# Kernel tuning notes

Measured on AMD Instinct MI355X. Metric: run time of the kernel, lower is better.

The kernel has to match this reference:

```python
import jax, jax.numpy as jnp
import numpy as np

NUM_HEADS = 16

def setup_inputs() -> dict:
    key = jax.random.key(0)
    k1, k2, k3 = jax.random.split(key, 3)
    T, B, E = 2048, 4, 1024
    x = jax.random.normal(k1, (T, B, E), dtype=jnp.float32)
    # xavier-ish scaled weights
    in_proj_w = jax.random.normal(k2, (3 * E, E), dtype=jnp.float32) * (1.0 / np.sqrt(E))
    in_proj_b = jnp.zeros((3 * E,), dtype=jnp.float32)
    out_w = jax.random.normal(k3, (E, E), dtype=jnp.float32) * (1.0 / np.sqrt(E))
    out_b = jnp.zeros((E,), dtype=jnp.float32)
    return {"x": x, "in_proj_w": in_proj_w, "in_proj_b": in_proj_b,
            "out_w": out_w, "out_b": out_b}

def reference(x, in_proj_w, in_proj_b, out_w, out_b):
    # Self-attention (query=key=value=x), shapes: x [T, B, E]
    T, B, E = x.shape
    H = NUM_HEADS
    D = E // H
    scaling = D ** -0.5
    # fused QKV projection: [T, B, 3E]
    qkv = jnp.einsum('tbe,fe->tbf', x, in_proj_w) + in_proj_b
    q, k, v = jnp.split(qkv, 3, axis=-1)
    q = q * scaling
    # [T, B, E] -> [B, H, T, D]
    def to_heads(t):
        return t.reshape(T, B, H, D).transpose(1, 2, 0, 3)
    q, k, v = to_heads(q), to_heads(k), to_heads(v)
    # scores [B, H, T, T], softmax in float32 as in the original
    scores = jnp.einsum('bhtd,bhsd->bhts', q, k)
    attn_weights = jax.nn.softmax(scores.astype(jnp.float32), axis=-1).astype(scores.dtype)
    # attn [B, H, T, D] -> [T, B, E]
    attn = jnp.einsum('bhts,bhsd->bhtd', attn_weights, v)
    attn = attn.transpose(2, 0, 1, 3).reshape(T, B, E)
    out = jnp.einsum('tbe,fe->tbf', attn, out_w) + out_b
    # averaged attention weights over heads: [B, T, T]
    avg_weights = attn_weights.sum(axis=1) / H
    return out, avg_weights
```

## Files before the change

### kernel.cpp

```cpp
#include <hip/hip_runtime.h>
#include <hip/hip_bf16.h>
#include <cstdint>
#include <cstddef>

typedef __attribute__((ext_vector_type(8))) short s16x8;
typedef __attribute__((ext_vector_type(4))) float f32x4;
typedef __attribute__((ext_vector_type(8))) float f32x8;
typedef __attribute__((ext_vector_type(8))) _Float16 h8;
typedef __attribute__((ext_vector_type(4))) _Float16 h4;

#define TT 2048
#define BB 4
#define EE 1024
#define HH 16
#define DD 64
#define MR 8192

#define MFMA_BF16(a,b,c) __builtin_amdgcn_mfma_f32_16x16x32_bf16(a,b,c,0,0,0)
#define MFMA_F16(a,b,c)  __builtin_amdgcn_mfma_f32_16x16x32_f16(a,b,c,0,0,0)

__device__ __forceinline__ ushort f2bf(float f) {
  uint32_t u = __float_as_uint(f);
  u += 0x7fffu + ((u >> 16) & 1u);
  return (ushort)(u >> 16);
}

#define GL2L(g, l) __builtin_amdgcn_global_load_lds( \
    (__attribute__((address_space(1))) void*)(g), \
    (__attribute__((address_space(3))) void*)(l), 16, 0, 0)

__global__ void cast_f32_bf16(const float* __restrict__ in, ushort* __restrict__ out, int n4) {
  int stride = gridDim.x * blockDim.x;
  for (int i = blockIdx.x * blockDim.x + threadIdx.x; i < n4; i += stride) {
    float4 v = ((const float4*)in)[i];
    ushort4 o;
    o.x = f2bf(v.x); o.y = f2bf(v.y); o.z = f2bf(v.z); o.w = f2bf(v.w);
    ((ushort4*)out)[i] = o;
  }
}

__global__ __launch_bounds__(256) void gemm_qkv(
    const ushort* __restrict__ A, const ushort* __restrict__ W,
    const float* __restrict__ bias,
    ushort* __restrict__ Qb, ushort* __restrict__ Kb, ushort* __restrict__ Vt)
{
  __shared__ ushort As[128 * 32];
  __shared__ ushort Bs[128 * 32];
  const int K = EE;
  int tid = threadIdx.x;
  int bn = blockIdx.x, bm = blockIdx.y;
  int brow = bm * 128, bcol = bn * 128;
  int lane = tid & 63, wid = tid >> 6;
  int wm = wid >> 1, wn = wid & 1;
  int lr = lane & 15, kg = lane >> 4;

  f32x4 zero = {0.f, 0.f, 0.f, 0.f};
  f32x4 acc[4][4];
#pragma unroll
  for (int i = 0; i < 4; i++)
#pragma unroll
    for (int j = 0; j < 4; j++) acc[i][j] = zero;

  int r0 = tid >> 2, c0 = (tid & 3) * 8;
  const ushort* Abase = A + (size_t)brow * K;
  const ushort* Wbase = W + (size_t)bcol * K;

  for (int k0 = 0; k0 < K; k0 += 32) {
    __syncthreads();
    GL2L(Abase + (size_t)r0 * K + k0 + c0,        &As[tid * 8]);
    GL2L(Abase + (size_t)(r0 + 64) * K + k0 + c0, &As[(tid + 256) * 8]);
    GL2L(Wbase + (size_t)r0 * K + k0 + c0,        &Bs[tid * 8]);
    GL2L(Wbase + (size_t)(r0 + 64) * K + k0 + c0, &Bs[(tid + 256) * 8]);
    __syncthreads();
    s16x8 af[4], bfr[4];
#pragma unroll
    for (int i = 0; i < 4; i++) af[i]  = *(const s16x8*)&As[(wm * 64 + i * 16 + lr) * 32 + kg * 8];
#pragma unroll
    for (int j = 0; j < 4; j++) bfr[j] = *(const s16x8*)&Bs[(wn * 64 + j * 16 + lr) * 32 + kg * 8];
#pragma unroll
    for (int i = 0; i < 4; i++)
#pragma unroll
      for (int j = 0; j < 4; j++)
        acc[i][j] = MFMA_BF16(af[i], bfr[j], acc[i][j]);
  }

#pragma unroll
  for (int i = 0; i < 4; i++)
#pragma unroll
    for (int j = 0; j < 4; j++) {
      int n = bcol + wn * 64 + j * 16 + lr;
      float bv = bias[n];
      int sec = n >> 10;
      int hd = n & 1023;
      int h = hd >> 6, d = hd & 63;
#pragma unroll
      for (int e = 0; e < 4; e++) {
        int m = brow + wm * 64 + i * 16 + kg * 4 + e;
        int t = m >> 2, b = m & 3;
        float v = acc[i][j][e] + bv;
        size_t hoff = (size_t)(b * HH + h);
        if (sec == 0)      Qb[(hoff * TT + t) * DD + d] = f2bf(v * 0.125f);
        else if (sec == 1) Kb[(hoff * TT + t) * DD + d] = f2bf(v);
        else { _Float16 hv = (_Float16)v; Vt[(hoff * DD + d) * TT + t] = *(ushort*)&hv; }
      }
    }
}

__global__ __launch_bounds__(512, 2) void attn_fused(
    const ushort* __restrict__ Qb, const ushort* __restrict__ Kb,
    const _Float16* __restrict__ Vt, ushort* __restrict__ attn,
    float* __restrict__ avgp)
{
  __shared__ _Float16 sc[32 * 2048];
  __shared__ float scr[2048];
  __shared__ float invl[32];

  const int qt = blockIdx.x;
  const int b  = blockIdx.y;
  const int tid = threadIdx.x;
  const int lane = tid & 63;
  const int w = tid >> 6;
  const int m = lane & 15;
  const int kq = lane >> 4;
  const int t0 = qt * 32;

  f32x8 av[4][4];
#pragma unroll
  for (int u = 0; u < 4; u++)
#pragma unroll
    for (int c = 0; c < 4; c++) av[u][c] = (f32x8)(0.f);

  for (int h = 0; h < HH; ++h) {
    const size_t bh = (size_t)b * HH + h;

    const ushort* qp = Qb + (bh * TT + t0) * DD;
    s16x8 q00 = *(const s16x8*)&qp[(size_t)m * DD + kq * 8];
    s16x8 q01 = *(const s16x8*)&qp[(size_t)m * DD + 32 + kq * 8];
    s16x8 q10 = *(const s16x8*)&qp[(size_t)(16 + m) * DD + kq * 8];
    s16x8 q11 = *(const s16x8*)&qp[(size_t)(16 + m) * DD + 32 + kq * 8];

    const ushort* kbase = Kb + bh * TT * DD;
#pragma unroll 4
    for (int i = 0; i < 16; ++i) {
      int nt = w * 16 + i;
      const ushort* kr = kbase + (size_t)(nt * 16 + m) * DD + kq * 8;
      s16x8 a0 = *(const s16x8*)kr;
      s16x8 a1 = *(const s16x8*)(kr + 32);
      f32x4 c0 = {0.f, 0.f, 0.f, 0.f}, c1 = {0.f, 0.f, 0.f, 0.f};
      c0 = MFMA_BF16(a0, q00, c0); c0 = MFMA_BF16(a1, q01, c0);
      c1 = MFMA_BF16(a0, q10, c1); c1 = MFMA_BF16(a1, q11, c1);
      int ksw = (nt * 16 + kq * 4) ^ ((m & 7) << 3);
      h4 p0, p1;
#pragma unroll
      for (int e = 0; e < 4; e++) { p0[e] = (_Float16)c0[e]; p1[e] = (_Float16)c1[e]; }
      *(h4*)&sc[(size_t)m * 2048 + ksw] = p0;
      *(h4*)&sc[(size_t)(16 + m) * 2048 + ksw] = p1;
    }
    __syncthreads();

#pragma unroll
    for (int u = 0; u < 4; ++u) {
      int r = w * 4 + u;
      _Float16* rp = &sc[(size_t)r * 2048];
      int xr = (r & 7) << 3;
      float mx = -3e38f;
      h8 v[4];
#pragma unroll
      for (int c = 0; c < 4; ++c) {
        v[c] = *(const h8*)&rp[((c * 64 + lane) * 8) ^ xr];
#pragma unroll
        for (int j = 0; j < 8; j++) mx = fmaxf(mx, (float)v[c][j]);
      }
#pragma unroll
      for (int o = 32; o; o >>= 1) mx = fmaxf(mx, __shfl_xor(mx, o));
      float l = 0.f;
      h8 ev[4];
#pragma unroll
      for (int c = 0; c < 4; ++c) {
#pragma unroll
        for (int j = 0; j < 8; j++) { float e = __expf((float)v[c][j] - mx); l += e; ev[c][j] = (_Float16)e; }
        *(h8*)&rp[((c * 64 + lane) * 8) ^ xr] = ev[c];
      }
#pragma unroll
      for (int o = 32; o; o >>= 1) l += __shfl_xor(l, o);
      float inv = 1.0f / l;
      if (lane == 0) invl[r] = inv;
#pragma unroll
      for (int c = 0; c < 4; ++c)
#pragma unroll
        for (int j = 0; j < 8; j++)
          av[u][c][j] += (float)ev[c][j] * inv;
    }
    __syncthreads();

    {
      int dtl = w & 3, kh = w >> 2;
      const _Float16* vb = Vt + bh * DD * TT + (size_t)(dtl * 16 + m) * TT + kh * 1024 + kq * 8;
      const _Float16* a0p = &sc[(size_t)m * 2048];
      const _Float16* a1p = &sc[(size_t)(16 + m) * 2048];
      int xr = (m & 7) << 3;
      f32x4 acc0 = {0.f, 0.f, 0.f, 0.f}, acc1 = {0.f, 0.f, 0.f, 0.f};
#pragma unroll 4
      for (int s = 0; s < 32; ++s) {
        int ksw = (kh * 1024 + s * 32 + kq * 8) ^ xr;
        h8 bv = *(const h8*)(vb + s * 32);
        h8 a0 = *(const h8*)&a0p[ksw];
        h8 a1 = *(const h8*)&a1p[ksw];
        acc0 = MFMA_F16(a0, bv, acc0);
        acc1 = MFMA_F16(a1, bv, acc1);
      }
      if (kh == 1) {
#pragma unroll
        for (int e = 0; e < 4; e++) {
          scr[(dtl * 2 + 0) * 256 + (kq * 4 + e) * 16 + m] = acc0[e];
          scr[(dtl * 2 + 1) * 256 + (kq * 4 + e) * 16 + m] = acc1[e];
        }
      }
      __syncthreads();
      if (kh == 0) {
#pragma unroll
        for (int e = 0; e < 4; e++) {
          int ql = kq * 4 + e;
          float v0 = (acc0[e] + scr[(dtl * 2 + 0) * 256 + ql * 16 + m]) * invl[ql];
          float v1 = (acc1[e] + scr[(dtl * 2 + 1) * 256 + ql * 16 + m]) * invl[16 + ql];
          attn[((size_t)(t0 + ql) * BB + b) * EE + h * DD + dtl * 16 + m] = f2bf(v0);
          attn[((size_t)(t0 + 16 + ql) * BB + b) * EE + h * DD + dtl * 16 + m] = f2bf(v1);
        }
      }
    }
    __syncthreads();
  }

#pragma unroll
  for (int u = 0; u < 4; ++u) {
    float* gp = avgp + ((size_t)b * TT + t0 + w * 4 + u) * TT;
#pragma unroll
    for (int c = 0; c < 4; ++c) {
      int cb = (c * 64 + lane) * 8;
      float4 o0 = {av[u][c][0] * 0.0625f, av[u][c][1] * 0.0625f,
                   av[u][c][2] * 0.0625f, av[u][c][3] * 0.0625f};
      float4 o1 = {av[u][c][4] * 0.0625f, av[u][c][5] * 0.0625f,
                   av[u][c][6] * 0.0625f, av[u][c][7] * 0.0625f};
      ((float4*)(gp + cb))[0] = o0;
      ((float4*)(gp + cb))[1] = o1;
    }
  }
}

__global__ __launch_bounds__(256) void gemm_out(
    const ushort* __restrict__ A, const ushort* __restrict__ W,
    const float* __restrict__ bias, float* __restrict__ out)
{
  __shared__ ushort As[128 * 32];
  __shared__ ushort Bs[128 * 32];
  const int K = EE;
  int tid = threadIdx.x;
  int bn = blockIdx.x, bm = blockIdx.y;
  int brow = bm * 128, bcol = bn * 128;
  int lane = tid & 63, wid = tid >> 6;
  int wm = wid >> 1, wn = wid & 1;
  int lr = lane & 15, kg = lane >> 4;

  f32x4 zero = {0.f, 0.f, 0.f, 0.f};
  f32x4 acc[4][4];
#pragma unroll
  for (int i = 0; i < 4; i++)
#pragma unroll
    for (int j = 0; j < 4; j++) acc[i][j] = zero;

  int r0 = tid >> 2, c0 = (tid & 3) * 8;
  const ushort* Abase = A + (size_t)brow * K;
  const ushort* Wbase = W + (size_t)bcol * K;

  for (int k0 = 0; k0 < K; k0 += 32) {
    __syncthreads();
    GL2L(Abase + (size_t)r0 * K + k0 + c0,        &As[tid * 8]);
    GL2L(Abase + (size_t)(r0 + 64) * K + k0 + c0, &As[(tid + 256) * 8]);
    GL2L(Wbase + (size_t)r0 * K + k0 + c0,        &Bs[tid * 8]);
    GL2L(Wbase + (size_t)(r0 + 64) * K + k0 + c0, &Bs[(tid + 256) * 8]);
    __syncthreads();
    s16x8 af[4], bfr[4];
#pragma unroll
    for (int i = 0; i < 4; i++) af[i]  = *(const s16x8*)&As[(wm * 64 + i * 16 + lr) * 32 + kg * 8];
#pragma unroll
    for (int j = 0; j < 4; j++) bfr[j] = *(const s16x8*)&Bs[(wn * 64 + j * 16 + lr) * 32 + kg * 8];
#pragma unroll
    for (int i = 0; i < 4; i++)
#pragma unroll
      for (int j = 0; j < 4; j++)
        acc[i][j] = MFMA_BF16(af[i], bfr[j], acc[i][j]);
  }

#pragma unroll
  for (int i = 0; i < 4; i++)
#pragma unroll
    for (int j = 0; j < 4; j++) {
      int n = bcol + wn * 64 + j * 16 + lr;
      float bv = bias[n];
#pragma unroll
      for (int e = 0; e < 4; e++) {
        int m = brow + wm * 64 + i * 16 + kg * 4 + e;
        out[(size_t)m * EE + n] = acc[i][j][e] + bv;
      }
    }
}

extern "C" void kernel_launch(void* const* d_in, const int* in_sizes, int n_in,
                              void* d_out, int out_size, void* d_ws, size_t ws_size,
                              hipStream_t stream) {
  const float* x  = (const float*)d_in[0];
  const float* w1 = (const float*)d_in[1];
  const float* b1 = (const float*)d_in[2];
  const float* w2 = (const float*)d_in[3];
  const float* b2 = (const float*)d_in[4];
  float* out = (float*)d_out;
  float* avg = out + (size_t)MR * EE;

  char* p = (char*)d_ws;
  ushort* Xb   = (ushort*)p; p += (size_t)MR * EE * 2;
  ushort* W1b  = (ushort*)p; p += (size_t)3 * EE * EE * 2;
  ushort* W2b  = (ushort*)p; p += (size_t)EE * EE * 2;
  ushort* Qb   = (ushort*)p; p += (size_t)BB * HH * TT * DD * 2;
  ushort* Kb   = (ushort*)p; p += (size_t)BB * HH * TT * DD * 2;
  ushort* Vt   = (ushort*)p; p += (size_t)BB * HH * TT * DD * 2;
  ushort* attn = (ushort*)p; p += (size_t)MR * EE * 2;
  (void)ws_size;

  cast_f32_bf16<<<1024, 256, 0, stream>>>(x,  Xb,  MR * EE / 4);
  cast_f32_bf16<<<512,  256, 0, stream>>>(w1, W1b, 3 * EE * EE / 4);
  cast_f32_bf16<<<256,  256, 0, stream>>>(w2, W2b, EE * EE / 4);
  gemm_qkv<<<dim3(24, 64), 256, 0, stream>>>(Xb, W1b, b1, Qb, Kb, Vt);
  attn_fused<<<dim3(TT / 32, BB), 512, 0, stream>>>(Qb, Kb, (const _Float16*)Vt, attn, avg);
  gemm_out<<<dim3(8, 64), 256, 0, stream>>>(attn, W2b, b2, out);
}
```

Before: 560.6 us.

## Compute row max in QK stage, fp16 head-average accumulators, split PV accumulators

The row maximum is now computed during the QK^T MFMA stage and combined through a small shared table, so the softmax pass no longer reads the score row twice. The per-thread head-averaged weight accumulators move from fp32 to fp16, which halves their register footprint. The PV loop uses two independent accumulator chains per output to expose more MFMA ILP, and the launch bound no longer requests two blocks per CU. The fp16 accumulation of the averaged weights over 16 heads loses precision, and dropping the occupancy hint may change how registers are allocated.

```diff
diff --git a/kernel.cpp b/kernel.cpp
--- a/kernel.cpp
+++ b/kernel.cpp
@@ -5,7 +5,6 @@
 
 typedef __attribute__((ext_vector_type(8))) short s16x8;
 typedef __attribute__((ext_vector_type(4))) float f32x4;
-typedef __attribute__((ext_vector_type(8))) float f32x8;
 typedef __attribute__((ext_vector_type(8))) _Float16 h8;
 typedef __attribute__((ext_vector_type(4))) _Float16 h4;
 
@@ -106,13 +105,14 @@
     }
 }
 
-__global__ __launch_bounds__(512, 2) void attn_fused(
+__global__ __launch_bounds__(512) void attn_fused(
     const ushort* __restrict__ Qb, const ushort* __restrict__ Kb,
     const _Float16* __restrict__ Vt, ushort* __restrict__ attn,
     float* __restrict__ avgp)
 {
   __shared__ _Float16 sc[32 * 2048];
   __shared__ float scr[2048];
+  __shared__ float pmax[32][8];
   __shared__ float invl[32];
 
   const int qt = blockIdx.x;
@@ -124,11 +124,13 @@
   const int kq = lane >> 4;
   const int t0 = qt * 32;
 
-  f32x8 av[4][4];
+  h8 av[4][4];
 #pragma unroll
   for (int u = 0; u < 4; u++)
 #pragma unroll
-    for (int c = 0; c < 4; c++) av[u][c] = (f32x8)(0.f);
+    for (int c = 0; c < 4; c++)
+#pragma unroll
+      for (int j = 0; j < 8; j++) av[u][c][j] = (_Float16)0.f;
 
   for (int h = 0; h < HH; ++h) {
     const size_t bh = (size_t)b * HH + h;
@@ -140,6 +142,7 @@
     s16x8 q11 = *(const s16x8*)&qp[(size_t)(16 + m) * DD + 32 + kq * 8];
 
     const ushort* kbase = Kb + bh * TT * DD;
+    float mx0 = -3e38f, mx1 = -3e38f;
 #pragma unroll 4
     for (int i = 0; i < 16; ++i) {
       int nt = w * 16 + i;
@@ -152,10 +155,16 @@
       int ksw = (nt * 16 + kq * 4) ^ ((m & 7) << 3);
       h4 p0, p1;
 #pragma unroll
-      for (int e = 0; e < 4; e++) { p0[e] = (_Float16)c0[e]; p1[e] = (_Float16)c1[e]; }
+      for (int e = 0; e < 4; e++) {
+        mx0 = fmaxf(mx0, c0[e]); mx1 = fmaxf(mx1, c1[e]);
+        p0[e] = (_Float16)c0[e]; p1[e] = (_Float16)c1[e];
+      }
       *(h4*)&sc[(size_t)m * 2048 + ksw] = p0;
       *(h4*)&sc[(size_t)(16 + m) * 2048 + ksw] = p1;
     }
+    mx0 = fmaxf(mx0, __shfl_xor(mx0, 16)); mx0 = fmaxf(mx0, __shfl_xor(mx0, 32));
+    mx1 = fmaxf(mx1, __shfl_xor(mx1, 16)); mx1 = fmaxf(mx1, __shfl_xor(mx1, 32));
+    if (lane < 16) { pmax[m][w] = mx0; pmax[16 + m][w] = mx1; }
     __syncthreads();
 
 #pragma unroll
@@ -164,32 +173,29 @@
       _Float16* rp = &sc[(size_t)r * 2048];
       int xr = (r & 7) << 3;
       float mx = -3e38f;
-      h8 v[4];
+#pragma unroll
+      for (int j = 0; j < 8; ++j) mx = fmaxf(mx, pmax[r][j]);
+      float l = 0.f;
+      h8 eh[4];
 #pragma unroll
       for (int c = 0; c < 4; ++c) {
-        v[c] = *(const h8*)&rp[((c * 64 + lane) * 8) ^ xr];
-#pragma unroll
-        for (int j = 0; j < 8; j++) mx = fmaxf(mx, (float)v[c][j]);
-      }
-#pragma unroll
-      for (int o = 32; o; o >>= 1) mx = fmaxf(mx, __shfl_xor(mx, o));
-      float l = 0.f;
-      h8 ev[4];
-#pragma unroll
-      for (int c = 0; c < 4; ++c) {
-#pragma unroll
-        for (int j = 0; j < 8; j++) { float e = __expf((float)v[c][j] - mx); l += e; ev[c][j] = (_Float16)e; }
-        *(h8*)&rp[((c * 64 + lane) * 8) ^ xr] = ev[c];
+        h8 t = *(const h8*)&rp[((c * 64 + lane) * 8) ^ xr];
+        h8 e;
+#pragma unroll
+        for (int j = 0; j < 8; j++) { float ef = __expf((float)t[j] - mx); l += ef; e[j] = (_Float16)ef; }
+        *(h8*)&rp[((c * 64 + lane) * 8) ^ xr] = e;
+        eh[c] = e;
       }
 #pragma unroll
       for (int o = 32; o; o >>= 1) l += __shfl_xor(l, o);
       float inv = 1.0f / l;
       if (lane == 0) invl[r] = inv;
+      _Float16 hinv = (_Float16)inv;
 #pragma unroll
       for (int c = 0; c < 4; ++c)
 #pragma unroll
         for (int j = 0; j < 8; j++)
-          av[u][c][j] += (float)ev[c][j] * inv;
+          av[u][c][j] += eh[c][j] * hinv;
     }
     __syncthreads();
 
@@ -199,21 +205,28 @@
       const _Float16* a0p = &sc[(size_t)m * 2048];
       const _Float16* a1p = &sc[(size_t)(16 + m) * 2048];
       int xr = (m & 7) << 3;
-      f32x4 acc0 = {0.f, 0.f, 0.f, 0.f}, acc1 = {0.f, 0.f, 0.f, 0.f};
-#pragma unroll 4
-      for (int s = 0; s < 32; ++s) {
-        int ksw = (kh * 1024 + s * 32 + kq * 8) ^ xr;
-        h8 bv = *(const h8*)(vb + s * 32);
-        h8 a0 = *(const h8*)&a0p[ksw];
-        h8 a1 = *(const h8*)&a1p[ksw];
-        acc0 = MFMA_F16(a0, bv, acc0);
-        acc1 = MFMA_F16(a1, bv, acc1);
+      f32x4 accA0 = {0.f, 0.f, 0.f, 0.f}, accB0 = {0.f, 0.f, 0.f, 0.f};
+      f32x4 accA1 = {0.f, 0.f, 0.f, 0.f}, accB1 = {0.f, 0.f, 0.f, 0.f};
+#pragma unroll 2
+      for (int s = 0; s < 32; s += 2) {
+        int ksw0 = (kh * 1024 + s * 32 + kq * 8) ^ xr;
+        int ksw1 = (kh * 1024 + (s + 1) * 32 + kq * 8) ^ xr;
+        h8 bv0 = *(const h8*)(vb + s * 32);
+        h8 bv1 = *(const h8*)(vb + (s + 1) * 32);
+        h8 a00 = *(const h8*)&a0p[ksw0];
+        h8 a01 = *(const h8*)&a0p[ksw1];
+        h8 a10 = *(const h8*)&a1p[ksw0];
+        h8 a11 = *(const h8*)&a1p[ksw1];
+        accA0 = MFMA_F16(a00, bv0, accA0);
+        accB0 = MFMA_F16(a01, bv1, accB0);
+        accA1 = MFMA_F16(a10, bv0, accA1);
+        accB1 = MFMA_F16(a11, bv1, accB1);
       }
       if (kh == 1) {
 #pragma unroll
         for (int e = 0; e < 4; e++) {
-          scr[(dtl * 2 + 0) * 256 + (kq * 4 + e) * 16 + m] = acc0[e];
-          scr[(dtl * 2 + 1) * 256 + (kq * 4 + e) * 16 + m] = acc1[e];
+          scr[(dtl * 2 + 0) * 256 + (kq * 4 + e) * 16 + m] = accA0[e] + accB0[e];
+          scr[(dtl * 2 + 1) * 256 + (kq * 4 + e) * 16 + m] = accA1[e] + accB1[e];
         }
       }
       __syncthreads();
@@ -221,8 +234,8 @@
 #pragma unroll
         for (int e = 0; e < 4; e++) {
           int ql = kq * 4 + e;
-          float v0 = (acc0[e] + scr[(dtl * 2 + 0) * 256 + ql * 16 + m]) * invl[ql];
-          float v1 = (acc1[e] + scr[(dtl * 2 + 1) * 256 + ql * 16 + m]) * invl[16 + ql];
+          float v0 = (accA0[e] + accB0[e] + scr[(dtl * 2 + 0) * 256 + ql * 16 + m]) * invl[ql];
+          float v1 = (accA1[e] + accB1[e] + scr[(dtl * 2 + 1) * 256 + ql * 16 + m]) * invl[16 + ql];
           attn[((size_t)(t0 + ql) * BB + b) * EE + h * DD + dtl * 16 + m] = f2bf(v0);
           attn[((size_t)(t0 + 16 + ql) * BB + b) * EE + h * DD + dtl * 16 + m] = f2bf(v1);
         }
@@ -237,10 +250,10 @@
 #pragma unroll
     for (int c = 0; c < 4; ++c) {
       int cb = (c * 64 + lane) * 8;
-      float4 o0 = {av[u][c][0] * 0.0625f, av[u][c][1] * 0.0625f,
-                   av[u][c][2] * 0.0625f, av[u][c][3] * 0.0625f};
-      float4 o1 = {av[u][c][4] * 0.0625f, av[u][c][5] * 0.0625f,
-                   av[u][c][6] * 0.0625f, av[u][c][7] * 0.0625f};
+      float4 o0 = {(float)av[u][c][0] * 0.0625f, (float)av[u][c][1] * 0.0625f,
+                   (float)av[u][c][2] * 0.0625f, (float)av[u][c][3] * 0.0625f};
+      float4 o1 = {(float)av[u][c][4] * 0.0625f, (float)av[u][c][5] * 0.0625f,
+                   (float)av[u][c][6] * 0.0625f, (float)av[u][c][7] * 0.0625f};
       ((float4*)(gp + cb))[0] = o0;
       ((float4*)(gp + cb))[1] = o1;
     }
```

After: 466.0 us, median of 3. 16.9% less time.
